# Optimization experiments

Hardware: AMD Instinct MI355X
Metric: run time of the kernel (lower is better)

## Reference

```python
import jax, jax.numpy as jnp
import numpy as np

N = 100000   # nodes
E = 1200000  # edges
D = 64       # feature / hidden dim (heads=1)
L = 3        # num_layers
G = 64       # num graphs
SCALE = 1.0 / np.sqrt(D)


def setup_inputs() -> dict:
    key = jax.random.key(0)
    ks = jax.random.split(key, 12)
    inp = {
        "x": jax.random.normal(ks[0], (N, D), dtype=jnp.float32),
        "edge_index": jax.random.randint(ks[1], (2, E), 0, N, dtype=jnp.int64),
        "batch": jnp.sort(jax.random.randint(ks[2], (N,), 0, G, dtype=jnp.int64)),
        "Wq": jax.random.normal(ks[3], (L, D, D), dtype=jnp.float32) * 0.1,
        "bq": jax.random.normal(ks[4], (L, D), dtype=jnp.float32) * 0.1,
        "Wk": jax.random.normal(ks[5], (L, D, D), dtype=jnp.float32) * 0.1,
        "bk": jax.random.normal(ks[6], (L, D), dtype=jnp.float32) * 0.1,
        "Wv": jax.random.normal(ks[7], (L, D, D), dtype=jnp.float32) * 0.1,
        "bv": jax.random.normal(ks[8], (L, D), dtype=jnp.float32) * 0.1,
        "Ws": jax.random.normal(ks[9], (L, D, D), dtype=jnp.float32) * 0.1,
        "bs": jax.random.normal(ks[10], (L, D), dtype=jnp.float32) * 0.1,
    }
    return inp


def _transformer_conv(x, src, dst, Wq, bq, Wk, bk, Wv, bv, Ws, bs):
    # PyG TransformerConv, heads=1, concat=True, root_weight=True, beta=False
    q = x @ Wq + bq            # [N, D] query of target nodes
    k = x @ Wk + bk            # [N, D] key of source nodes
    v = x @ Wv + bv            # [N, D] value of source nodes
    logits = jnp.sum(q[dst] * k[src], axis=-1) * SCALE  # [E]
    # segment softmax over incoming edges of each target node
    m = jax.ops.segment_max(logits, dst, num_segments=N)        # [N]
    e = jnp.exp(logits - m[dst])                                 # [E]
    denom = jax.ops.segment_sum(e, dst, num_segments=N)         # [N]
    alpha = e / denom[dst]                                       # [E]
    agg = jax.ops.segment_sum(alpha[:, None] * v[src], dst, num_segments=N)  # [N, D]
    return agg + x @ Ws + bs   # root/skip connection


def reference(x, edge_index, batch, Wq, bq, Wk, bk, Wv, bv, Ws, bs):
    src, dst = edge_index[0], edge_index[1]
    for l in range(L):
        x = _transformer_conv(x, src, dst, Wq[l], bq[l], Wk[l], bk[l],
                              Wv[l], bv[l], Ws[l], bs[l])
        x = jax.nn.relu(x)
    # global_mean_pool
    sums = jax.ops.segment_sum(x, batch, num_segments=G)                  # [G, D]
    counts = jax.ops.segment_sum(jnp.ones((N,), x.dtype), batch, num_segments=G)
    graph_emb = sums / jnp.maximum(counts, 1.0)[:, None]
    return (x, graph_emb)
```

## Files before the change

kernel.cpp:

```cpp
#include <hip/hip_runtime.h>
#include <math.h>

#define DD 64

typedef _Float16 h2 __attribute__((ext_vector_type(2)));
typedef _Float16 h4 __attribute__((ext_vector_type(4)));
typedef _Float16 h8 __attribute__((ext_vector_type(8)));
typedef float f32x4 __attribute__((ext_vector_type(4)));

__global__ __launch_bounds__(64) void k_wconv(
    const float* __restrict__ Wq, const float* __restrict__ Wk,
    const float* __restrict__ Wv, const float* __restrict__ Ws,
    _Float16* __restrict__ wf)
{
  int bid = blockIdx.x;
  int layer = bid >> 5;
  int c = (bid >> 1) & 15;
  int s = bid & 1;
  int lane = threadIdx.x;
  int col = c * 16 + (lane & 15);
  int mi = col >> 6;
  const float* W = (mi == 0 ? Wq : mi == 1 ? Wk : mi == 2 ? Wv : Ws)
                   + (size_t)layer * DD * DD;
  int colw = col & 63;
  _Float16* o = wf + ((((size_t)(layer * 16 + c)) * 2 + s) * 64 + lane) * 8;
  #pragma unroll
  for (int j = 0; j < 8; ++j) {
    int k = s * 32 + (lane >> 4) * 8 + j;
    o[j] = (_Float16)W[k * DD + colw];
  }
}

__global__ __launch_bounds__(256) void k_xconv(
    const float* __restrict__ x, _Float16* __restrict__ xb, int total8)
{
  int i = blockIdx.x * 256 + threadIdx.x;
  if (i >= total8) return;
  float4 a = ((const float4*)x)[i * 2];
  float4 b = ((const float4*)x)[i * 2 + 1];
  h8 o;
  o[0] = (_Float16)a.x; o[1] = (_Float16)a.y; o[2] = (_Float16)a.z; o[3] = (_Float16)a.w;
  o[4] = (_Float16)b.x; o[5] = (_Float16)b.y; o[6] = (_Float16)b.z; o[7] = (_Float16)b.w;
  *(h8*)(xb + (size_t)i * 8) = o;
}

#define LH_STRIDE 200
#define LF_STRIDE 68
#define WAVE_LDS  (16 * 400 + 16 * 272)

__global__ __launch_bounds__(256) void k_projM(
    const _Float16* __restrict__ xb, const _Float16* __restrict__ wf,
    const float* __restrict__ bq, const float* __restrict__ bk,
    const float* __restrict__ bv, const float* __restrict__ bs,
    _Float16* __restrict__ qh, _Float16* __restrict__ kvh,
    float* __restrict__ sout, int n)
{
  __shared__ __align__(16) char lds[4 * WAVE_LDS];
  int wave = threadIdx.x >> 6;
  int lane = threadIdx.x & 63;
  int nbase = blockIdx.x * 64 + wave * 16;
  if (nbase >= n) return;

  char* wbase = lds + wave * WAVE_LDS;
  _Float16* lh = (_Float16*)wbase;
  float*    lf = (float*)(wbase + 16 * 400);

  const int cl = lane & 15;
  const int rq = lane >> 4;

  int ar = min(nbase + cl, n - 1);
  h8 a0 = *(const h8*)(xb + (size_t)ar * DD + rq * 8);
  h8 a1 = *(const h8*)(xb + (size_t)ar * DD + 32 + rq * 8);

  #pragma unroll
  for (int c = 0; c < 16; ++c) {
    const float* bp = (c < 4) ? bq : (c < 8) ? bk : (c < 12) ? bv : bs;
    const int fb = c * 16 + rq * 4;
    float4 b4 = *(const float4*)(bp + (fb & 63));
    f32x4 acc; acc[0] = b4.x; acc[1] = b4.y; acc[2] = b4.z; acc[3] = b4.w;
    const _Float16* wp = wf + ((size_t)(c * 2) * 64 + lane) * 8;
    h8 w0 = *(const h8*)(wp);
    h8 w1 = *(const h8*)(wp + 64 * 8);
    acc = __builtin_amdgcn_mfma_f32_16x16x32_f16(w0, a0, acc, 0, 0, 0);
    acc = __builtin_amdgcn_mfma_f32_16x16x32_f16(w1, a1, acc, 0, 0, 0);

    if (c < 12) {
      h4 o; o[0] = (_Float16)acc[0]; o[1] = (_Float16)acc[1];
      o[2] = (_Float16)acc[2]; o[3] = (_Float16)acc[3];
      *(h4*)(lh + cl * LH_STRIDE + fb) = o;
    } else {
      *(f32x4*)(lf + cl * LF_STRIDE + (fb - 192)) = acc;
    }
  }

  #pragma unroll
  for (int i = 0; i < 2; ++i) {
    int chunk = i * 64 + lane;
    int nd = chunk >> 3, co = chunk & 7;
    h8 v = *(const h8*)(lh + nd * LH_STRIDE + co * 8);
    if (nbase + nd < n)
      *(h8*)(qh + (size_t)(nbase + nd) * DD + co * 8) = v;
  }
  #pragma unroll
  for (int i = 0; i < 4; ++i) {
    int chunk = i * 64 + lane;
    int nd = chunk >> 4, co = chunk & 15;
    h8 v = *(const h8*)(lh + nd * LH_STRIDE + 64 + co * 8);
    if (nbase + nd < n)
      *(h8*)(kvh + (size_t)(nbase + nd) * 128 + co * 8) = v;
  }
  #pragma unroll
  for (int i = 0; i < 4; ++i) {
    int chunk = i * 64 + lane;
    int nd = chunk >> 4, co = chunk & 15;
    f32x4 v = *(const f32x4*)(lf + nd * LF_STRIDE + co * 4);
    if (nbase + nd < n)
      *(f32x4*)(sout + (size_t)(nbase + nd) * DD + co * 4) = v;
  }
}

__global__ __launch_bounds__(256) void k_hist(
    const int* __restrict__ dst, int* __restrict__ deg,
    unsigned short* __restrict__ pos, int ecnt)
{
  int e = (blockIdx.x * 256 + threadIdx.x) * 4;
  if (e + 3 < ecnt) {
    int4 d = *(const int4*)(dst + e);
    pos[e]     = (unsigned short)atomicAdd(deg + d.x, 1);
    pos[e + 1] = (unsigned short)atomicAdd(deg + d.y, 1);
    pos[e + 2] = (unsigned short)atomicAdd(deg + d.z, 1);
    pos[e + 3] = (unsigned short)atomicAdd(deg + d.w, 1);
  } else {
    for (; e < ecnt; ++e)
      pos[e] = (unsigned short)atomicAdd(deg + dst[e], 1);
  }
}

__global__ __launch_bounds__(1024) void k_scanA(
    const int* __restrict__ deg, int* __restrict__ rowptr,
    int* __restrict__ btot, int* __restrict__ dbins, int n)
{
  __shared__ int wsum[16];
  __shared__ int lbin[256];
  int tid = threadIdx.x;
  int lane = tid & 63, wave = tid >> 6;
  if (tid < 256) lbin[tid] = 0;
  __syncthreads();
  int i = blockIdx.x * 4096 + tid * 4;
  int4 d = make_int4(0, 0, 0, 0);
  if (i + 3 < n) d = *(const int4*)(deg + i);
  else {
    if (i     < n) d.x = deg[i];
    if (i + 1 < n) d.y = deg[i + 1];
    if (i + 2 < n) d.z = deg[i + 2];
  }
  if (i     < n) atomicAdd(&lbin[min(d.x, 255)], 1);
  if (i + 1 < n) atomicAdd(&lbin[min(d.y, 255)], 1);
  if (i + 2 < n) atomicAdd(&lbin[min(d.z, 255)], 1);
  if (i + 3 < n) atomicAdd(&lbin[min(d.w, 255)], 1);

  int s1 = d.x, s2 = s1 + d.y, s3 = s2 + d.z, s4 = s3 + d.w;
  int s = s4;
  #pragma unroll
  for (int off = 1; off < 64; off <<= 1) {
    int t = __shfl_up(s, off);
    if (lane >= off) s += t;
  }
  if (lane == 63) wsum[wave] = s;
  __syncthreads();
  if (wave == 0) {
    int ws = (lane < 16) ? wsum[lane] : 0;
    #pragma unroll
    for (int off = 1; off < 16; off <<= 1) {
      int t = __shfl_up(ws, off);
      if (lane >= off) ws += t;
    }
    if (lane < 16) wsum[lane] = ws;
  }
  __syncthreads();
  int excl = ((wave > 0) ? wsum[wave - 1] : 0) + s - s4;
  if (i     < n) rowptr[i + 1] = excl + s1;
  if (i + 1 < n) rowptr[i + 2] = excl + s2;
  if (i + 2 < n) rowptr[i + 3] = excl + s3;
  if (i + 3 < n) rowptr[i + 4] = excl + s4;
  if (tid == 0) {
    if (blockIdx.x == 0) rowptr[0] = 0;
    btot[blockIdx.x] = wsum[15];
  }
  if (tid < 256 && lbin[tid]) atomicAdd(&dbins[tid], lbin[tid]);
}

__global__ __launch_bounds__(64) void k_scanB(
    int* __restrict__ btot, int nb, const int* __restrict__ dbins,
    int* __restrict__ dcur)
{
  int lane = threadIdx.x;
  int v = (lane < nb) ? btot[lane] : 0;
  int s = v;
  #pragma unroll
  for (int off = 1; off < 64; off <<= 1) {
    int t = __shfl_up(s, off);
    if (lane >= off) s += t;
  }
  if (lane < nb) btot[lane] = s - v;

  int4 dv = *(const int4*)(dbins + lane * 4);
  int t1 = dv.x, t2 = t1 + dv.y, t3 = t2 + dv.z, t4 = t3 + dv.w;
  int ss = t4;
  #pragma unroll
  for (int off = 1; off < 64; off <<= 1) {
    int t = __shfl_up(ss, off);
    if (lane >= off) ss += t;
  }
  int ex = ss - t4;
  dcur[lane * 4]     = ex;
  dcur[lane * 4 + 1] = ex + t1;
  dcur[lane * 4 + 2] = ex + t2;
  dcur[lane * 4 + 3] = ex + t3;
}

__global__ __launch_bounds__(1024) void k_scanC(
    int* __restrict__ rowptr, const int* __restrict__ btot, int n)
{
  int off = btot[blockIdx.x];
  if (off == 0) return;
  int i = blockIdx.x * 4096 + threadIdx.x * 4;
  #pragma unroll
  for (int k = 1; k <= 4; ++k)
    if (i + k <= n) rowptr[i + k] += off;
}

__global__ __launch_bounds__(1024) void k_dfill(
    const int* __restrict__ deg, int* __restrict__ dcur,
    int* __restrict__ order, int n)
{
  __shared__ int lcnt[256];
  __shared__ int lbase[256];
  int tid = threadIdx.x;
  if (tid < 256) lcnt[tid] = 0;
  __syncthreads();
  int i = blockIdx.x * 1024 + tid;
  int b = 0, slot = 0;
  bool ok = (i < n);
  if (ok) {
    b = min(deg[i], 255);
    slot = atomicAdd(&lcnt[b], 1);
  }
  __syncthreads();
  if (tid < 256 && lcnt[tid]) lbase[tid] = atomicAdd(&dcur[tid], lcnt[tid]);
  __syncthreads();
  if (ok) order[lbase[b] + slot] = i;
}

__global__ __launch_bounds__(256) void k_fill(
    const int* __restrict__ src, const int* __restrict__ dst,
    const int* __restrict__ rowptr, const unsigned short* __restrict__ pos,
    int* __restrict__ adj, int ecnt)
{
  int e = (blockIdx.x * 256 + threadIdx.x) * 4;
  if (e + 3 < ecnt) {
    int4 d = *(const int4*)(dst + e);
    int4 s = *(const int4*)(src + e);
    ushort4 p = *(const ushort4*)(pos + e);
    adj[rowptr[d.x] + p.x] = s.x;
    adj[rowptr[d.y] + p.y] = s.y;
    adj[rowptr[d.z] + p.z] = s.z;
    adj[rowptr[d.w] + p.w] = s.w;
  } else {
    for (; e < ecnt; ++e)
      adj[rowptr[dst[e]] + pos[e]] = src[e];
  }
}

#define H2OF(v, i) __builtin_shufflevector((v), (v), 2*(i), 2*(i)+1)

template<bool LAST>
__global__ __launch_bounds__(256) void k_node(
    const _Float16* __restrict__ qh, const _Float16* __restrict__ kvh,
    const int* __restrict__ rowptr, const int* __restrict__ adj,
    const int* __restrict__ order,
    const float* __restrict__ sskip, float* __restrict__ outp,
    _Float16* __restrict__ xbnext, int n)
{
  int wid = (blockIdx.x * blockDim.x + threadIdx.x) >> 6;
  int lane = threadIdx.x & 63;
  const int g = lane >> 3;
  const int t = lane & 7;

  int idx = wid * 8 + g;
  bool nok = (idx < n);
  int node = order[nok ? idx : (n - 1)];

  const h8 q8 = *(const h8*)(qh + (size_t)node * DD + t * 8);
  const h2 qp0 = H2OF(q8, 0), qp1 = H2OF(q8, 1), qp2 = H2OF(q8, 2), qp3 = H2OF(q8, 3);

  const int e0 = rowptr[node];
  const int d  = nok ? (rowptr[node + 1] - e0) : 0;

  int dm = d;
  dm = max(dm, __shfl_xor(dm, 8));
  dm = max(dm, __shfl_xor(dm, 16));
  dm = max(dm, __shfl_xor(dm, 32));

  float mg = -1e30f, den = 0.f;
  float agg[8] = {0.f, 0.f, 0.f, 0.f, 0.f, 0.f, 0.f, 0.f};

  const char* kvb = (const char*)kvh;
  h8 kP, vP;
  if (d > 0) {
    int s = adj[e0];
    unsigned off = ((unsigned)s << 8) + ((unsigned)t << 4);
    kP = *(const h8*)(kvb + off);
    vP = *(const h8*)(kvb + off + 128);
  }

  for (int it = 0; it < dm; ++it) {
    const h8 kc = kP, vc = vP;
    const bool valid = (it < d);
    if (it + 1 < d) {
      int s2 = adj[e0 + it + 1];
      unsigned off = ((unsigned)s2 << 8) + ((unsigned)t << 4);
      kP = *(const h8*)(kvb + off);
      vP = *(const h8*)(kvb + off + 128);
    }

#if __has_builtin(__builtin_amdgcn_fdot2)
    float p = __builtin_amdgcn_fdot2(qp0, H2OF(kc, 0), 0.f, false);
    p = __builtin_amdgcn_fdot2(qp1, H2OF(kc, 1), p, false);
    p = __builtin_amdgcn_fdot2(qp2, H2OF(kc, 2), p, false);
    p = __builtin_amdgcn_fdot2(qp3, H2OF(kc, 3), p, false);
#else
    h2 ph = qp0 * H2OF(kc, 0);
    ph = qp1 * H2OF(kc, 1) + ph;
    ph = qp2 * H2OF(kc, 2) + ph;
    ph = qp3 * H2OF(kc, 3) + ph;
    float p = (float)ph.x + (float)ph.y;
#endif
    p += __shfl_xor(p, 1);
    p += __shfl_xor(p, 2);
    p += __shfl_xor(p, 4);
    p *= 0.125f;

    if (valid && p > mg) {
      float c = __expf(mg - p);
      den *= c;
      #pragma unroll
      for (int j = 0; j < 8; ++j) agg[j] *= c;
      mg = p;
    }
    float w = valid ? __expf(p - mg) : 0.f;
    den += w;
    #pragma unroll
    for (int j = 0; j < 8; ++j)
      agg[j] = fmaf(w, (float)vc[j], agg[j]);
  }

  if (nok) {
    float inv = (den > 0.f) ? (1.0f / den) : 0.f;
    const float* sp = sskip + (size_t)node * DD + t * 8;
    float4 sa = *(const float4*)(sp);
    float4 sb = *(const float4*)(sp + 4);
    float r[8];
    r[0] = fmaxf(fmaf(agg[0], inv, sa.x), 0.f);
    r[1] = fmaxf(fmaf(agg[1], inv, sa.y), 0.f);
    r[2] = fmaxf(fmaf(agg[2], inv, sa.z), 0.f);
    r[3] = fmaxf(fmaf(agg[3], inv, sa.w), 0.f);
    r[4] = fmaxf(fmaf(agg[4], inv, sb.x), 0.f);
    r[5] = fmaxf(fmaf(agg[5], inv, sb.y), 0.f);
    r[6] = fmaxf(fmaf(agg[6], inv, sb.z), 0.f);
    r[7] = fmaxf(fmaf(agg[7], inv, sb.w), 0.f);
    if (LAST) {
      float* op = outp + (size_t)node * DD + t * 8;
      *(float4*)(op)     = make_float4(r[0], r[1], r[2], r[3]);
      *(float4*)(op + 4) = make_float4(r[4], r[5], r[6], r[7]);
    } else {
      h8 xh;
      #pragma unroll
      for (int j = 0; j < 8; ++j) xh[j] = (_Float16)r[j];
      *(h8*)(xbnext + (size_t)node * DD + t * 8) = xh;
    }
  }
}

__global__ __launch_bounds__(64) void k_pool_sum(
    const float* __restrict__ x, const int* __restrict__ batch,
    float* __restrict__ gsum, float* __restrict__ gcnt, int n)
{
  int lane = threadIdx.x;
  int n0 = blockIdx.x * 64;
  if (n0 >= n) return;
  int n1 = min(n0 + 64, n);
  float acc = 0.f;
  int g_prev = batch[n0];
  int run = 0;
  for (int nn = n0; nn < n1; ++nn) {
    int g = batch[nn];
    if (g != g_prev) {
      atomicAdd(gsum + (size_t)g_prev * DD + lane, acc);
      if (lane == 0) atomicAdd(gcnt + g_prev, (float)run);
      acc = 0.f; run = 0; g_prev = g;
    }
    acc += x[(size_t)nn * DD + lane];
    run++;
  }
  atomicAdd(gsum + (size_t)g_prev * DD + lane, acc);
  if (lane == 0) atomicAdd(gcnt + g_prev, (float)run);
}

__global__ __launch_bounds__(256) void k_pool_div(
    const float* __restrict__ gsum, const float* __restrict__ gcnt,
    float* __restrict__ emb, int gtot)
{
  int gid = blockIdx.x * blockDim.x + threadIdx.x;
  if (gid >= gtot * DD) return;
  int g = gid >> 6;
  emb[gid] = gsum[gid] / fmaxf(gcnt[g], 1.0f);
}

extern "C" void kernel_launch(void* const* d_in, const int* in_sizes, int n_in,
                              void* d_out, int out_size, void* d_ws, size_t ws_size,
                              hipStream_t stream)
{
  const float* x_in  = (const float*)d_in[0];
  const int*   ei    = (const int*)  d_in[1];
  const int*   batch = (const int*)  d_in[2];
  const float* Wq = (const float*)d_in[3];
  const float* bq = (const float*)d_in[4];
  const float* Wk = (const float*)d_in[5];
  const float* bk = (const float*)d_in[6];
  const float* Wv = (const float*)d_in[7];
  const float* bv = (const float*)d_in[8];
  const float* Ws = (const float*)d_in[9];
  const float* bs = (const float*)d_in[10];

  const int nd     = in_sizes[0];
  const int n      = nd / DD;
  const int ecnt   = in_sizes[1] / 2;
  const int layers = in_sizes[3] / (DD * DD);
  const int gtot   = (out_size - nd) / DD;

  const int* src = ei;
  const int* dst = ei + ecnt;

  char* cur = (char*)d_ws;
  float*     P0  = (float*)cur;     cur += (size_t)nd * 4;
  _Float16*  XB  = (_Float16*)cur;  cur += (size_t)nd * 2;
  _Float16*  QH  = (_Float16*)cur;  cur += (size_t)nd * 2;
  _Float16*  KVH = (_Float16*)cur;  cur += (size_t)nd * 4;
  _Float16*  WF  = (_Float16*)cur;  cur += (size_t)layers * 16384 * 2;
  int* rowptr = (int*)cur;          cur += (size_t)(n + 4) * 4;
  int* adj    = (int*)cur;          cur += (size_t)(ecnt + 8) * 4;
  int* deg    = (int*)cur;          cur += (size_t)n * 4;
  int* dbins  = (int*)cur;          cur += 256 * 4;
  int* dcur   = (int*)cur;          cur += 256 * 4;
  int* btot   = (int*)cur;          cur += 64 * 4;
  int* order  = (int*)cur;          cur += (size_t)n * 4;
  unsigned short* pos = (unsigned short*)cur; cur += (size_t)ecnt * 2;
  float* gsum = (float*)cur;        cur += (size_t)gtot * DD * 4;
  float* gcnt = (float*)cur;

  float* out = (float*)d_out;

  k_wconv<<<layers * 32, 64, 0, stream>>>(Wq, Wk, Wv, Ws, WF);
  k_xconv<<<(n * 8 + 255) / 256, 256, 0, stream>>>(x_in, XB, n * 8);
  hipMemsetAsync(deg, 0, (size_t)(n + 256) * 4, stream);
  const int eb4 = (ecnt + 1023) / 1024;
  k_hist<<<eb4, 256, 0, stream>>>(dst, deg, pos, ecnt);
  const int nbk = (n + 4095) / 4096;
  k_scanA<<<nbk, 1024, 0, stream>>>(deg, rowptr, btot, dbins, n);
  k_scanB<<<1, 64, 0, stream>>>(btot, nbk, dbins, dcur);
  k_scanC<<<nbk, 1024, 0, stream>>>(rowptr, btot, n);
  k_dfill<<<(n + 1023) / 1024, 1024, 0, stream>>>(deg, dcur, order, n);
  k_fill<<<eb4, 256, 0, stream>>>(src, dst, rowptr, pos, adj, ecnt);

  const int pj = (n + 63) / 64;
  const int nb = (n + 31) / 32;

  for (int l = 0; l < layers; ++l) {
    const size_t bo = (size_t)l * DD;
    k_projM<<<pj, 256, 0, stream>>>(XB, WF + (size_t)l * 16384,
                                    bq + bo, bk + bo, bv + bo, bs + bo,
                                    QH, KVH, P0, n);
    if (l == layers - 1)
      k_node<true><<<nb, 256, 0, stream>>>(QH, KVH, rowptr, adj, order,
                                           P0, out, XB, n);
    else
      k_node<false><<<nb, 256, 0, stream>>>(QH, KVH, rowptr, adj, order,
                                            P0, out, XB, n);
  }

  hipMemsetAsync(gsum, 0, (size_t)(gtot * DD + gtot) * 4, stream);
  const int pbk = (n + 63) / 64;
  k_pool_sum<<<pbk, 64, 0, stream>>>(out, batch, gsum, gcnt, n);
  const int fb = (gtot * DD + 255) / 256;
  k_pool_div<<<fb, 256, 0, stream>>>(gsum, gcnt, out + (size_t)nd, gtot);
}
```

Baseline: 350.7 us.

## Fuse prep/scan kernels, store skip in fp16, fuse pooling into last node kernel

```diff
diff --git a/kernel.cpp b/kernel.cpp
--- a/kernel.cpp
+++ b/kernel.cpp
@@ -2,58 +2,60 @@
 #include <math.h>
 
 #define DD 64
+#define APAD 512
 
 typedef _Float16 h2 __attribute__((ext_vector_type(2)));
 typedef _Float16 h4 __attribute__((ext_vector_type(4)));
 typedef _Float16 h8 __attribute__((ext_vector_type(8)));
 typedef float f32x4 __attribute__((ext_vector_type(4)));
 
-__global__ __launch_bounds__(64) void k_wconv(
+__global__ __launch_bounds__(256) void k_prep(
     const float* __restrict__ Wq, const float* __restrict__ Wk,
     const float* __restrict__ Wv, const float* __restrict__ Ws,
-    _Float16* __restrict__ wf)
-{
-  int bid = blockIdx.x;
-  int layer = bid >> 5;
-  int c = (bid >> 1) & 15;
-  int s = bid & 1;
-  int lane = threadIdx.x;
-  int col = c * 16 + (lane & 15);
-  int mi = col >> 6;
-  const float* W = (mi == 0 ? Wq : mi == 1 ? Wk : mi == 2 ? Wv : Ws)
-                   + (size_t)layer * DD * DD;
-  int colw = col & 63;
-  _Float16* o = wf + ((((size_t)(layer * 16 + c)) * 2 + s) * 64 + lane) * 8;
-  #pragma unroll
-  for (int j = 0; j < 8; ++j) {
-    int k = s * 32 + (lane >> 4) * 8 + j;
-    o[j] = (_Float16)W[k * DD + colw];
-  }
-}
-
-__global__ __launch_bounds__(256) void k_xconv(
-    const float* __restrict__ x, _Float16* __restrict__ xb, int total8)
-{
-  int i = blockIdx.x * 256 + threadIdx.x;
-  if (i >= total8) return;
-  float4 a = ((const float4*)x)[i * 2];
-  float4 b = ((const float4*)x)[i * 2 + 1];
-  h8 o;
-  o[0] = (_Float16)a.x; o[1] = (_Float16)a.y; o[2] = (_Float16)a.z; o[3] = (_Float16)a.w;
-  o[4] = (_Float16)b.x; o[5] = (_Float16)b.y; o[6] = (_Float16)b.z; o[7] = (_Float16)b.w;
-  *(h8*)(xb + (size_t)i * 8) = o;
+    _Float16* __restrict__ wf,
+    const float* __restrict__ x, _Float16* __restrict__ xb,
+    int wblocks, int total8)
+{
+  int tid = threadIdx.x;
+  if ((int)blockIdx.x < wblocks) {
+    int id = blockIdx.x * 4 + (tid >> 6);
+    int lane = tid & 63;
+    int layer = id >> 5;
+    int c = (id >> 1) & 15;
+    int s = id & 1;
+    int col = c * 16 + (lane & 15);
+    int mi = col >> 6;
+    const float* W = (mi == 0 ? Wq : mi == 1 ? Wk : mi == 2 ? Wv : Ws)
+                     + (size_t)layer * DD * DD;
+    int colw = col & 63;
+    _Float16* o = wf + ((((size_t)(layer * 16 + c)) * 2 + s) * 64 + lane) * 8;
+    #pragma unroll
+    for (int j = 0; j < 8; ++j) {
+      int k = s * 32 + (lane >> 4) * 8 + j;
+      o[j] = (_Float16)W[k * DD + colw];
+    }
+  } else {
+    int i = (blockIdx.x - wblocks) * 256 + tid;
+    if (i >= total8) return;
+    float4 a = ((const float4*)x)[i * 2];
+    float4 b = ((const float4*)x)[i * 2 + 1];
+    h8 o;
+    o[0] = (_Float16)a.x; o[1] = (_Float16)a.y; o[2] = (_Float16)a.z; o[3] = (_Float16)a.w;
+    o[4] = (_Float16)b.x; o[5] = (_Float16)b.y; o[6] = (_Float16)b.z; o[7] = (_Float16)b.w;
+    *(h8*)(xb + (size_t)i * 8) = o;
+  }
 }
 
 #define LH_STRIDE 200
-#define LF_STRIDE 68
-#define WAVE_LDS  (16 * 400 + 16 * 272)
+#define LS_STRIDE 72
+#define WAVE_LDS  (16 * 400 + 16 * 144)
 
 __global__ __launch_bounds__(256) void k_projM(
     const _Float16* __restrict__ xb, const _Float16* __restrict__ wf,
     const float* __restrict__ bq, const float* __restrict__ bk,
     const float* __restrict__ bv, const float* __restrict__ bs,
     _Float16* __restrict__ qh, _Float16* __restrict__ kvh,
-    float* __restrict__ sout, int n)
+    _Float16* __restrict__ sh, int n)
 {
   __shared__ __align__(16) char lds[4 * WAVE_LDS];
   int wave = threadIdx.x >> 6;
@@ -63,7 +65,7 @@
 
   char* wbase = lds + wave * WAVE_LDS;
   _Float16* lh = (_Float16*)wbase;
-  float*    lf = (float*)(wbase + 16 * 400);
+  _Float16* ls = (_Float16*)(wbase + 16 * 400);
 
   const int cl = lane & 15;
   const int rq = lane >> 4;
@@ -84,13 +86,12 @@
     acc = __builtin_amdgcn_mfma_f32_16x16x32_f16(w0, a0, acc, 0, 0, 0);
     acc = __builtin_amdgcn_mfma_f32_16x16x32_f16(w1, a1, acc, 0, 0, 0);
 
-    if (c < 12) {
-      h4 o; o[0] = (_Float16)acc[0]; o[1] = (_Float16)acc[1];
-      o[2] = (_Float16)acc[2]; o[3] = (_Float16)acc[3];
+    h4 o; o[0] = (_Float16)acc[0]; o[1] = (_Float16)acc[1];
+    o[2] = (_Float16)acc[2]; o[3] = (_Float16)acc[3];
+    if (c < 12)
       *(h4*)(lh + cl * LH_STRIDE + fb) = o;
-    } else {
-      *(f32x4*)(lf + cl * LF_STRIDE + (fb - 192)) = acc;
-    }
+    else
+      *(h4*)(ls + cl * LS_STRIDE + (fb - 192)) = o;
   }
 
   #pragma unroll
@@ -110,12 +111,12 @@
       *(h8*)(kvh + (size_t)(nbase + nd) * 128 + co * 8) = v;
   }
   #pragma unroll
-  for (int i = 0; i < 4; ++i) {
+  for (int i = 0; i < 2; ++i) {
     int chunk = i * 64 + lane;
-    int nd = chunk >> 4, co = chunk & 15;
-    f32x4 v = *(const f32x4*)(lf + nd * LF_STRIDE + co * 4);
+    int nd = chunk >> 3, co = chunk & 7;
+    h8 v = *(const h8*)(ls + nd * LS_STRIDE + co * 8);
     if (nbase + nd < n)
-      *(f32x4*)(sout + (size_t)(nbase + nd) * DD + co * 4) = v;
+      *(h8*)(sh + (size_t)(nbase + nd) * DD + co * 8) = v;
   }
 }
 
@@ -219,37 +220,37 @@
   dcur[lane * 4 + 3] = ex + t3;
 }
 
-__global__ __launch_bounds__(1024) void k_scanC(
-    int* __restrict__ rowptr, const int* __restrict__ btot, int n)
-{
-  int off = btot[blockIdx.x];
-  if (off == 0) return;
-  int i = blockIdx.x * 4096 + threadIdx.x * 4;
-  #pragma unroll
-  for (int k = 1; k <= 4; ++k)
-    if (i + k <= n) rowptr[i + k] += off;
-}
-
-__global__ __launch_bounds__(1024) void k_dfill(
+__global__ __launch_bounds__(1024) void k_scanCD(
+    int* __restrict__ rowptr, const int* __restrict__ btot,
     const int* __restrict__ deg, int* __restrict__ dcur,
-    int* __restrict__ order, int n)
+    int* __restrict__ order, int n, int nbk)
 {
   __shared__ int lcnt[256];
   __shared__ int lbase[256];
   int tid = threadIdx.x;
+  int b = blockIdx.x;
+  if (b < nbk) {
+    int off = btot[b];
+    if (off) {
+      int i = b * 4096 + tid * 4;
+      #pragma unroll
+      for (int k = 1; k <= 4; ++k)
+        if (i + k <= n) rowptr[i + k] += off;
+    }
+  }
   if (tid < 256) lcnt[tid] = 0;
   __syncthreads();
-  int i = blockIdx.x * 1024 + tid;
-  int b = 0, slot = 0;
+  int i = b * 1024 + tid;
+  int bin = 0, slot = 0;
   bool ok = (i < n);
   if (ok) {
-    b = min(deg[i], 255);
-    slot = atomicAdd(&lcnt[b], 1);
+    bin = min(deg[i], 255);
+    slot = atomicAdd(&lcnt[bin], 1);
   }
   __syncthreads();
   if (tid < 256 && lcnt[tid]) lbase[tid] = atomicAdd(&dcur[tid], lcnt[tid]);
   __syncthreads();
-  if (ok) order[lbase[b] + slot] = i;
+  if (ok) order[(n - 1) - (lbase[bin] + slot)] = i;
 }
 
 __global__ __launch_bounds__(256) void k_fill(
@@ -279,8 +280,9 @@
     const _Float16* __restrict__ qh, const _Float16* __restrict__ kvh,
     const int* __restrict__ rowptr, const int* __restrict__ adj,
     const int* __restrict__ order,
-    const float* __restrict__ sskip, float* __restrict__ outp,
-    _Float16* __restrict__ xbnext, int n)
+    const _Float16* __restrict__ sh, float* __restrict__ outp,
+    _Float16* __restrict__ xbnext,
+    const int* __restrict__ batch, float* __restrict__ gsum, int n)
 {
   int wid = (blockIdx.x * blockDim.x + threadIdx.x) >> 6;
   int lane = threadIdx.x & 63;
@@ -306,10 +308,12 @@
   float agg[8] = {0.f, 0.f, 0.f, 0.f, 0.f, 0.f, 0.f, 0.f};
 
   const char* kvb = (const char*)kvh;
+  const unsigned tb = (unsigned)t << 4;
+
   h8 kP, vP;
-  if (d > 0) {
+  {
     int s = adj[e0];
-    unsigned off = ((unsigned)s << 8) + ((unsigned)t << 4);
+    unsigned off = ((unsigned)s << 8) + tb;
     kP = *(const h8*)(kvb + off);
     vP = *(const h8*)(kvb + off + 128);
   }
@@ -317,9 +321,9 @@
   for (int it = 0; it < dm; ++it) {
     const h8 kc = kP, vc = vP;
     const bool valid = (it < d);
-    if (it + 1 < d) {
+    {
       int s2 = adj[e0 + it + 1];
-      unsigned off = ((unsigned)s2 << 8) + ((unsigned)t << 4);
+      unsigned off = ((unsigned)s2 << 8) + tb;
       kP = *(const h8*)(kvb + off);
       vP = *(const h8*)(kvb + off + 128);
     }
@@ -357,22 +361,19 @@
 
   if (nok) {
     float inv = (den > 0.f) ? (1.0f / den) : 0.f;
-    const float* sp = sskip + (size_t)node * DD + t * 8;
-    float4 sa = *(const float4*)(sp);
-    float4 sb = *(const float4*)(sp + 4);
+    const h8 s8 = *(const h8*)(sh + (size_t)node * DD + t * 8);
     float r[8];
-    r[0] = fmaxf(fmaf(agg[0], inv, sa.x), 0.f);
-    r[1] = fmaxf(fmaf(agg[1], inv, sa.y), 0.f);
-    r[2] = fmaxf(fmaf(agg[2], inv, sa.z), 0.f);
-    r[3] = fmaxf(fmaf(agg[3], inv, sa.w), 0.f);
-    r[4] = fmaxf(fmaf(agg[4], inv, sb.x), 0.f);
-    r[5] = fmaxf(fmaf(agg[5], inv, sb.y), 0.f);
-    r[6] = fmaxf(fmaf(agg[6], inv, sb.z), 0.f);
-    r[7] = fmaxf(fmaf(agg[7], inv, sb.w), 0.f);
+    #pragma unroll
+    for (int j = 0; j < 8; ++j)
+      r[j] = fmaxf(fmaf(agg[j], inv, (float)s8[j]), 0.f);
     if (LAST) {
       float* op = outp + (size_t)node * DD + t * 8;
       *(float4*)(op)     = make_float4(r[0], r[1], r[2], r[3]);
       *(float4*)(op + 4) = make_float4(r[4], r[5], r[6], r[7]);
+      int gb = batch[node];
+      float* gp = gsum + (size_t)gb * DD + t * 8;
+      #pragma unroll
+      for (int j = 0; j < 8; ++j) atomicAdd(gp + j, r[j]);
     } else {
       h8 xh;
       #pragma unroll
@@ -382,39 +383,25 @@
   }
 }
 
-__global__ __launch_bounds__(64) void k_pool_sum(
-    const float* __restrict__ x, const int* __restrict__ batch,
-    float* __restrict__ gsum, float* __restrict__ gcnt, int n)
-{
-  int lane = threadIdx.x;
-  int n0 = blockIdx.x * 64;
-  if (n0 >= n) return;
-  int n1 = min(n0 + 64, n);
-  float acc = 0.f;
-  int g_prev = batch[n0];
-  int run = 0;
-  for (int nn = n0; nn < n1; ++nn) {
-    int g = batch[nn];
-    if (g != g_prev) {
-      atomicAdd(gsum + (size_t)g_prev * DD + lane, acc);
-      if (lane == 0) atomicAdd(gcnt + g_prev, (float)run);
-      acc = 0.f; run = 0; g_prev = g;
-    }
-    acc += x[(size_t)nn * DD + lane];
-    run++;
-  }
-  atomicAdd(gsum + (size_t)g_prev * DD + lane, acc);
-  if (lane == 0) atomicAdd(gcnt + g_prev, (float)run);
+__device__ __forceinline__ int lbound(const int* __restrict__ a, int n, int key)
+{
+  int lo = 0, hi = n;
+  while (lo < hi) {
+    int mid = (lo + hi) >> 1;
+    if (a[mid] < key) lo = mid + 1; else hi = mid;
+  }
+  return lo;
 }
 
 __global__ __launch_bounds__(256) void k_pool_div(
-    const float* __restrict__ gsum, const float* __restrict__ gcnt,
-    float* __restrict__ emb, int gtot)
+    const float* __restrict__ gsum, const int* __restrict__ batch,
+    float* __restrict__ emb, int gtot, int n)
 {
   int gid = blockIdx.x * blockDim.x + threadIdx.x;
   if (gid >= gtot * DD) return;
   int g = gid >> 6;
-  emb[gid] = gsum[gid] / fmaxf(gcnt[g], 1.0f);
+  int cnt = lbound(batch, n, g + 1) - lbound(batch, n, g);
+  emb[gid] = gsum[gid] / fmaxf((float)cnt, 1.0f);
 }
 
 extern "C" void kernel_launch(void* const* d_in, const int* in_sizes, int n_in,
@@ -443,13 +430,13 @@
   const int* dst = ei + ecnt;
 
   char* cur = (char*)d_ws;
-  float*     P0  = (float*)cur;     cur += (size_t)nd * 4;
+  _Float16*  SH  = (_Float16*)cur;  cur += (size_t)nd * 2;
   _Float16*  XB  = (_Float16*)cur;  cur += (size_t)nd * 2;
   _Float16*  QH  = (_Float16*)cur;  cur += (size_t)nd * 2;
   _Float16*  KVH = (_Float16*)cur;  cur += (size_t)nd * 4;
   _Float16*  WF  = (_Float16*)cur;  cur += (size_t)layers * 16384 * 2;
   int* rowptr = (int*)cur;          cur += (size_t)(n + 4) * 4;
-  int* adj    = (int*)cur;          cur += (size_t)(ecnt + 8) * 4;
+  int* adj    = (int*)cur;          cur += (size_t)(ecnt + APAD) * 4;
   int* deg    = (int*)cur;          cur += (size_t)n * 4;
   int* dbins  = (int*)cur;          cur += 256 * 4;
   int* dcur   = (int*)cur;          cur += 256 * 4;
@@ -457,20 +444,22 @@
   int* order  = (int*)cur;          cur += (size_t)n * 4;
   unsigned short* pos = (unsigned short*)cur; cur += (size_t)ecnt * 2;
   float* gsum = (float*)cur;        cur += (size_t)gtot * DD * 4;
-  float* gcnt = (float*)cur;
 
   float* out = (float*)d_out;
 
-  k_wconv<<<layers * 32, 64, 0, stream>>>(Wq, Wk, Wv, Ws, WF);
-  k_xconv<<<(n * 8 + 255) / 256, 256, 0, stream>>>(x_in, XB, n * 8);
-  hipMemsetAsync(deg, 0, (size_t)(n + 256) * 4, stream);
+  const int wblocks = layers * 8;
+  const int xblocks = (n * 8 + 255) / 256;
+  k_prep<<<wblocks + xblocks, 256, 0, stream>>>(Wq, Wk, Wv, Ws, WF,
+                                                x_in, XB, wblocks, n * 8);
+  hipMemsetAsync(adj + ecnt, 0, (size_t)(APAD + n + 256) * 4, stream);
+  hipMemsetAsync(gsum, 0, (size_t)gtot * DD * 4, stream);
   const int eb4 = (ecnt + 1023) / 1024;
   k_hist<<<eb4, 256, 0, stream>>>(dst, deg, pos, ecnt);
   const int nbk = (n + 4095) / 4096;
   k_scanA<<<nbk, 1024, 0, stream>>>(deg, rowptr, btot, dbins, n);
   k_scanB<<<1, 64, 0, stream>>>(btot, nbk, dbins, dcur);
-  k_scanC<<<nbk, 1024, 0, stream>>>(rowptr, btot, n);
-  k_dfill<<<(n + 1023) / 1024, 1024, 0, stream>>>(deg, dcur, order, n);
+  const int dblk = (n + 1023) / 1024;
+  k_scanCD<<<dblk, 1024, 0, stream>>>(rowptr, btot, deg, dcur, order, n, nbk);
   k_fill<<<eb4, 256, 0, stream>>>(src, dst, rowptr, pos, adj, ecnt);
 
   const int pj = (n + 63) / 64;
@@ -480,18 +469,15 @@
     const size_t bo = (size_t)l * DD;
     k_projM<<<pj, 256, 0, stream>>>(XB, WF + (size_t)l * 16384,
                                     bq + bo, bk + bo, bv + bo, bs + bo,
-                                    QH, KVH, P0, n);
+                                    QH, KVH, SH, n);
     if (l == layers - 1)
       k_node<true><<<nb, 256, 0, stream>>>(QH, KVH, rowptr, adj, order,
-                                           P0, out, XB, n);
+                                           SH, out, XB, batch, gsum, n);
     else
       k_node<false><<<nb, 256, 0, stream>>>(QH, KVH, rowptr, adj, order,
-                                            P0, out, XB, n);
-  }
-
-  hipMemsetAsync(gsum, 0, (size_t)(gtot * DD + gtot) * 4, stream);
-  const int pbk = (n + 63) / 64;
-  k_pool_sum<<<pbk, 64, 0, stream>>>(out, batch, gsum, gcnt, n);
+                                            SH, out, XB, batch, gsum, n);
+  }
+
   const int fb = (gtot * DD + 255) / 256;
-  k_pool_div<<<fb, 256, 0, stream>>>(gsum, gcnt, out + (size_t)nd, gtot);
-}
+  k_pool_div<<<fb, 256, 0, stream>>>(gsum, batch, out + (size_t)nd, gtot, n);
+}
```

New measurement: 799.2 us. +127.9%, slower.
